# Kernel optimization log

Measured on AMD Instinct MI355X. Metric: run time of the kernel, lower is better.

## Reference

```python
import jax, jax.numpy as jnp
import numpy as np

N = 8192       # nodes == in_channels (diff matrix is NxN)
DF = 256       # feature dim of z
E = 65536      # edges (unused by forward, kept for signature fidelity)
M = 4096       # len(reliable_negatives)
NEG = 10       # neg_samples
STEPS = 10     # num_diffusion_steps
TEMP = 0.2


def setup_inputs() -> dict:
    key = jax.random.key(0)
    k1, k2, k3, k4, k5 = jax.random.split(key, 5)
    z = jax.random.normal(k1, (N, DF), dtype=jnp.float32)
    # learned parameter; init positive-uniform so row sums are well conditioned
    diff_matrix = jax.random.uniform(k2, (N, N), dtype=jnp.float32)
    edge_index = jax.random.randint(k3, (2, E), 0, N)
    reliable_negatives = jax.random.randint(k4, (M,), 0, N)
    # deterministic stand-in for torch.randint(0, len(reliable_negatives), (neg_samples,))
    neg_idx = jax.random.randint(k5, (NEG,), 0, M)
    return {"z": z, "diff_matrix": diff_matrix, "edge_index": edge_index,
            "reliable_negatives": reliable_negatives, "neg_idx": neg_idx}


def _l2norm(x):
    # F.normalize(dim=1): divide by L2 norm clamped at 1e-12
    n = jnp.sqrt(jnp.sum(x * x, axis=1, keepdims=True))
    return x / jnp.maximum(n, 1e-12)


def reference(z, diff_matrix, edge_index, reliable_negatives, neg_idx):
    # 10-step loop: mm(inverse(diag(rowsum)), M) == row-wise reciprocal scaling
    dm = diff_matrix
    for _ in range(STEPS):
        dm = dm / jnp.sum(dm, axis=1, keepdims=True)  # [N, N]
    # (normalized_diff_matrix with +eps*I is computed in the original but unused)

    anchor = z                       # [N, DF]
    positive = dm @ z                # [N, DF] diffused features
    negative = z[neg_idx]            # [NEG, DF]

    a = _l2norm(anchor)
    p = _l2norm(positive)
    n = _l2norm(negative)

    pos_sim = jnp.sum(a * p, axis=1) / TEMP                 # [N]
    neg_sim = jnp.exp(jnp.einsum('nd,kd->nk', a, n) / TEMP)  # [N, NEG]
    loss = -jnp.log(jnp.exp(pos_sim) / (jnp.exp(pos_sim) + neg_sim.sum(axis=1))).mean()
    return loss
```

## Files before the change

kernel.cpp:

```cpp
#include <hip/hip_runtime.h>
#include <hip/hip_bf16.h>


typedef float f32x4 __attribute__((ext_vector_type(4)));
typedef short s16x8 __attribute__((ext_vector_type(8)));

#define NN 8192
#define DFF 256
#define NNEG 10

__device__ __forceinline__ unsigned short f2bf(float x) {
  return __builtin_bit_cast(unsigned short, __float2bfloat16(x));
}

__device__ __forceinline__ float bf2f(unsigned short u) {
  return __builtin_bit_cast(float, (unsigned int)u << 16);
}

__device__ __forceinline__ void gload_lds16(const void* g, void* l) {
  __builtin_amdgcn_global_load_lds(
      (const __attribute__((address_space(1))) void*)(void*)g,
      (__attribute__((address_space(3))) void*)l, 16, 0, 0);
}

__device__ __forceinline__ float dot4(float4 a, float4 b) {
  return a.x * b.x + a.y * b.y + a.z * b.z + a.w * b.w;
}

__global__ void k_pack(const float* __restrict__ z,
                       unsigned short* __restrict__ zp) {
  __shared__ float tile[64][65];
  const int bx = blockIdx.x;
  const int by = blockIdx.y;
  const int t = threadIdx.x;
  const int lc = t & 63, lq = t >> 6;
#pragma unroll
  for (int p = 0; p < 16; ++p) {
    const int kr = lq * 16 + p;
    tile[kr][lc] = z[(size_t)(bx * 64 + kr) * DFF + by * 64 + lc];
  }
  __syncthreads();
#pragma unroll
  for (int p2 = 0; p2 < 2; ++p2) {
    const int ko = lq * 2 + p2;
    s16x8 v;
#pragma unroll
    for (int ke = 0; ke < 8; ++ke) v[ke] = (short)f2bf(tile[ko * 8 + ke][lc]);
    const int chunk = bx * 2 + (ko >> 2);
    const int kw = ko & 3;
    const int d = by * 64 + lc;
    *(s16x8*)(zp + (size_t)chunk * 8192 + kw * 2048 + d * 8) = v;
  }
}

__global__ __launch_bounds__(1024, 1) void k_gemm(const float* __restrict__ dm,
                                                  const unsigned short* __restrict__ zp,
                                                  unsigned short* __restrict__ part,
                                                  int KS) {
  __shared__ __align__(16) unsigned short sA[2][8192];
  __shared__ __align__(16) unsigned short sB[2][8192];
  const int bx = blockIdx.x;
  const int ks = bx & (KS - 1);
  const int mtile = bx / KS;
  const int klen = NN / KS;
  const int k0 = ks * klen;
  const int c0 = k0 >> 5;
  const int steps = klen / 32;
  const int tid = threadIdx.x;
  const int w = tid >> 6;
  const int l = tid & 63;
  const int m0 = mtile * 256;

  const int arow = tid >> 2;
  const int akw = tid & 3;
  const float* asrc = dm + (size_t)(m0 + arow) * NN + k0 + akw * 8;

  const int r16 = l & 15, kw = l >> 4;
  const int wm = w >> 2, wn = w & 3;

  f32x4 acc[4][4] = {};
  f32x4 a0, a1;

#define LOAD_A(t_)                                                           \
  {                                                                          \
    a0 = *(const f32x4*)(asrc + (t_)*32);                                    \
    a1 = *(const f32x4*)(asrc + (t_)*32 + 4);                                \
  }

#define WRITE_A(s_)                                                         \
  {                                                                         \
    s16x8 h_;                                                               \
    h_[0] = (short)f2bf(a0[0]); h_[1] = (short)f2bf(a0[1]);                 \
    h_[2] = (short)f2bf(a0[2]); h_[3] = (short)f2bf(a0[3]);                 \
    h_[4] = (short)f2bf(a1[0]); h_[5] = (short)f2bf(a1[1]);                 \
    h_[6] = (short)f2bf(a1[2]); h_[7] = (short)f2bf(a1[3]);                 \
    *(s16x8*)&sA[s_][akw * 2048 + arow * 8] = h_;                           \
  }

#define STAGE_B(t_, s_)                                                     \
  {                                                                         \
    const unsigned short* cs_ = zp + (size_t)(c0 + (t_)) * 8192;            \
    gload_lds16((const char*)(cs_ + w * 512) + l * 16,                      \
                (char*)sB[s_] + w * 1024);                                  \
  }

#define COMPUTE(s_)                                                         \
  {                                                                         \
    s16x8 af[4], bfr[4];                                                    \
    _Pragma("unroll") for (int mi = 0; mi < 4; ++mi) {                      \
      const int row_ = wm * 64 + mi * 16 + r16;                             \
      af[mi] = *(const s16x8*)&sA[s_][kw * 2048 + row_ * 8];                \
    }                                                                       \
    _Pragma("unroll") for (int nj = 0; nj < 4; ++nj) {                      \
      const int col_ = wn * 64 + nj * 16 + r16;                             \
      bfr[nj] = *(const s16x8*)&sB[s_][kw * 2048 + col_ * 8];               \
    }                                                                       \
    _Pragma("unroll") for (int mi = 0; mi < 4; ++mi)                        \
      _Pragma("unroll") for (int nj = 0; nj < 4; ++nj)                      \
        acc[mi][nj] = __builtin_amdgcn_mfma_f32_16x16x32_bf16(              \
            af[mi], bfr[nj], acc[mi][nj], 0, 0, 0);                         \
  }

  STAGE_B(0, 0);
  LOAD_A(0);
  WRITE_A(0);
  __syncthreads();

  for (int t = 0; t < steps; ++t) {
    const int cur = t & 1, nxt = cur ^ 1;
    if (t + 1 < steps) {
      LOAD_A(t + 1);
      STAGE_B(t + 1, nxt);
    }
    COMPUTE(cur);
    if (t + 1 < steps) WRITE_A(nxt);
    __syncthreads();
  }

#undef LOAD_A
#undef WRITE_A
#undef STAGE_B
#undef COMPUTE

  unsigned short* cb = part + (size_t)ks * NN * DFF;
#pragma unroll
  for (int mi = 0; mi < 4; ++mi)
#pragma unroll
    for (int nj = 0; nj < 4; ++nj) {
      const int col = wn * 64 + nj * 16 + r16;
      const int row0 = m0 + wm * 64 + mi * 16 + kw * 4;
#pragma unroll
      for (int r = 0; r < 4; ++r)
        cb[(size_t)(row0 + r) * DFF + col] = f2bf(acc[mi][nj][r]);
    }
}

__global__ __launch_bounds__(256) void k_loss(const float* __restrict__ z,
                                              const unsigned short* __restrict__ part,
                                              const int* __restrict__ neg_idx,
                                              float* __restrict__ lpart, int KS) {
  __shared__ float sneg[NNEG * DFF];
  __shared__ float swsum[4];
  const int t = threadIdx.x;
  const int w = t >> 6, l = t & 63;
  for (int k = w; k < NNEG; k += 4) {
    const int idx = neg_idx[k];
    float4 v = *(const float4*)(z + (size_t)idx * DFF + l * 4);
    float ss = dot4(v, v);
#pragma unroll
    for (int off = 32; off > 0; off >>= 1) ss += __shfl_xor(ss, off);
    const float s = 1.0f / fmaxf(sqrtf(ss), 1e-12f);
    float4 o;
    o.x = v.x * s; o.y = v.y * s; o.z = v.z * s; o.w = v.w * s;
    *(float4*)&sneg[k * DFF + l * 4] = o;
  }
  __syncthreads();
  const int gw = blockIdx.x * 4 + w;
  float lsum = 0.f;
  for (int rr = 0; rr < 8; ++rr) {
    const int i = gw * 8 + rr;
    const float4 a = *(const float4*)(z + (size_t)i * DFF + l * 4);
    float4 p; p.x = 0.f; p.y = 0.f; p.z = 0.f; p.w = 0.f;
    for (int ksp = 0; ksp < KS; ++ksp) {
      const ushort4 q =
          *(const ushort4*)(part + ((size_t)ksp * NN + i) * DFF + l * 4);
      p.x += bf2f(q.x); p.y += bf2f(q.y); p.z += bf2f(q.z); p.w += bf2f(q.w);
    }
    float vals[13];
    vals[0] = dot4(a, a);
    vals[1] = dot4(p, p);
    vals[2] = dot4(a, p);
#pragma unroll
    for (int k = 0; k < NNEG; ++k) {
      const float4 nv = *(const float4*)&sneg[k * DFF + l * 4];
      vals[3 + k] = dot4(a, nv);
    }
#pragma unroll
    for (int off = 32; off > 0; off >>= 1)
#pragma unroll
      for (int j = 0; j < 13; ++j) vals[j] += __shfl_xor(vals[j], off);
    const float na = fmaxf(sqrtf(vals[0]), 1e-12f);
    const float npp = fmaxf(sqrtf(vals[1]), 1e-12f);
    const float ps = vals[2] / (na * npp) * 5.0f;
    float S = 0.f;
#pragma unroll
    for (int k = 0; k < NNEG; ++k) S += expf(vals[3 + k] / na * 5.0f);
    lsum += logf(expf(ps) + S) - ps;
  }
  if (l == 0) swsum[w] = lsum;
  __syncthreads();
  if (t == 0) lpart[blockIdx.x] = swsum[0] + swsum[1] + swsum[2] + swsum[3];
}

__global__ void k_final(const float* __restrict__ lpart, float* __restrict__ out) {
  const int t = threadIdx.x;
  float v = lpart[t] + lpart[t + 64] + lpart[t + 128] + lpart[t + 192];
#pragma unroll
  for (int off = 32; off > 0; off >>= 1) v += __shfl_xor(v, off);
  if (t == 0) out[0] = v * (1.0f / (float)NN);
}

extern "C" void kernel_launch(void* const* d_in, const int* in_sizes, int n_in,
                              void* d_out, int out_size, void* d_ws, size_t ws_size,
                              hipStream_t stream) {
  const float* z = (const float*)d_in[0];
  const float* dm = (const float*)d_in[1];
  const int* neg_idx = (const int*)d_in[4];
  float* out = (float*)d_out;

  const size_t ZP = (size_t)NN * DFF * 2;
  auto need = [ZP](size_t ks) { return ZP + ks * (size_t)NN * DFF * 2 + 1024; };
  int KS = 8;
  if (ws_size < need(8)) KS = (ws_size >= need(4)) ? 4 : 2;

  char* ws = (char*)d_ws;
  unsigned short* zp = (unsigned short*)ws;
  unsigned short* part = (unsigned short*)(ws + ZP);
  float* lpart = (float*)(ws + ZP + (size_t)KS * NN * DFF * 2);

  k_pack<<<dim3(128, 4), 256, 0, stream>>>(z, zp);
  k_gemm<<<32 * KS, 1024, 0, stream>>>(dm, zp, part, KS);
  k_loss<<<256, 256, 0, stream>>>(z, part, neg_idx, lpart, KS);
  k_final<<<1, 64, 0, stream>>>(lpart, out);
}
```

Baseline: 130.9 us.

## Halve GEMM M-tile and assign K-splits per XCC via atomic work counter

The GEMM block tile shrinks from 256 to 128 rows with 512 threads and two blocks per CU, doubling the grid. Each block now takes its (mtile, k-split) from an atomic counter keyed by the hardware XCC id, so blocks on the same XCC tend to share the same K slice of the packed z operand and reuse it in that XCC's L2. The counters are zeroed in the pack kernel. This adds an atomic and a barrier at block start, and a fallback path that can give duplicate or missing tiles if counters overflow under odd scheduling.

```diff
diff --git a/kernel.cpp b/kernel.cpp
--- a/kernel.cpp
+++ b/kernel.cpp
@@ -28,7 +28,10 @@
 }
 
 __global__ void k_pack(const float* __restrict__ z,
-                       unsigned short* __restrict__ zp) {
+                       unsigned short* __restrict__ zp,
+                       unsigned int* __restrict__ cnt) {
+  if (blockIdx.x == 0 && blockIdx.y == 0 && threadIdx.x < 16)
+    cnt[threadIdx.x] = 0u;
   __shared__ float tile[64][65];
   const int bx = blockIdx.x;
   const int by = blockIdx.y;
@@ -53,15 +56,30 @@
   }
 }
 
-__global__ __launch_bounds__(1024, 1) void k_gemm(const float* __restrict__ dm,
-                                                  const unsigned short* __restrict__ zp,
-                                                  unsigned short* __restrict__ part,
-                                                  int KS) {
-  __shared__ __align__(16) unsigned short sA[2][8192];
+__global__ __launch_bounds__(512, 2) void k_gemm(const float* __restrict__ dm,
+                                                 const unsigned short* __restrict__ zp,
+                                                 unsigned short* __restrict__ part,
+                                                 unsigned int* __restrict__ cnt,
+                                                 int KS) {
+  __shared__ __align__(16) unsigned short sA[2][4096];
   __shared__ __align__(16) unsigned short sB[2][8192];
-  const int bx = blockIdx.x;
-  const int ks = bx & (KS - 1);
-  const int mtile = bx / KS;
+  __shared__ int s_mt, s_ks;
+  if (threadIdx.x == 0) {
+    unsigned int xcc;
+    asm volatile("s_getreg_b32 %0, hwreg(HW_REG_XCC_ID)" : "=s"(xcc));
+    xcc &= 7u;
+    int mt = 0, kk = 0;
+    for (int tr = 0; tr < 8; ++tr) {
+      const int k2 = (int)((xcc + (unsigned)tr) % (unsigned)KS);
+      const unsigned int o = atomicAdd(&cnt[k2], 1u);
+      if (o < 64u) { mt = (int)o; kk = k2; break; }
+    }
+    s_mt = mt;
+    s_ks = kk;
+  }
+  __syncthreads();
+  const int mtile = s_mt;
+  const int ks = s_ks;
   const int klen = NN / KS;
   const int k0 = ks * klen;
   const int c0 = k0 >> 5;
@@ -69,10 +87,10 @@
   const int tid = threadIdx.x;
   const int w = tid >> 6;
   const int l = tid & 63;
-  const int m0 = mtile * 256;
-
-  const int arow = tid >> 2;
-  const int akw = tid & 3;
+  const int m0 = mtile * 128;
+
+  const int arow = w * 16 + (l & 15);
+  const int akw = l >> 4;
   const float* asrc = dm + (size_t)(m0 + arow) * NN + k0 + akw * 8;
 
   const int r16 = l & 15, kw = l >> 4;
@@ -94,14 +112,17 @@
     h_[2] = (short)f2bf(a0[2]); h_[3] = (short)f2bf(a0[3]);                 \
     h_[4] = (short)f2bf(a1[0]); h_[5] = (short)f2bf(a1[1]);                 \
     h_[6] = (short)f2bf(a1[2]); h_[7] = (short)f2bf(a1[3]);                 \
-    *(s16x8*)&sA[s_][akw * 2048 + arow * 8] = h_;                           \
+    *(s16x8*)&sA[s_][akw * 1024 + arow * 8] = h_;                           \
   }
 
 #define STAGE_B(t_, s_)                                                     \
   {                                                                         \
     const unsigned short* cs_ = zp + (size_t)(c0 + (t_)) * 8192;            \
-    gload_lds16((const char*)(cs_ + w * 512) + l * 16,                      \
-                (char*)sB[s_] + w * 1024);                                  \
+    _Pragma("unroll") for (int q = 0; q < 2; ++q) {                         \
+      const int piece_ = w * 2 + q;                    \
+      gload_lds16((const char*)(cs_ + piece_ * 512) + l * 16,               \
+                  (char*)sB[s_] + piece_ * 1024);                           \
+    }                                                                       \
   }
 
 #define COMPUTE(s_)                                                         \
@@ -109,7 +130,7 @@
     s16x8 af[4], bfr[4];                                                    \
     _Pragma("unroll") for (int mi = 0; mi < 4; ++mi) {                      \
       const int row_ = wm * 64 + mi * 16 + r16;                             \
-      af[mi] = *(const s16x8*)&sA[s_][kw * 2048 + row_ * 8];                \
+      af[mi] = *(const s16x8*)&sA[s_][kw * 1024 + row_ * 8];                \
     }                                                                       \
     _Pragma("unroll") for (int nj = 0; nj < 4; ++nj) {                      \
       const int col_ = wn * 64 + nj * 16 + r16;                             \
@@ -229,7 +250,9 @@
   float* out = (float*)d_out;
 
   const size_t ZP = (size_t)NN * DFF * 2;
-  auto need = [ZP](size_t ks) { return ZP + ks * (size_t)NN * DFF * 2 + 1024; };
+  auto need = [ZP](size_t ks) {
+    return ZP + ks * (size_t)NN * DFF * 2 + 1024 + 64;
+  };
   int KS = 8;
   if (ws_size < need(8)) KS = (ws_size >= need(4)) ? 4 : 2;
 
@@ -237,9 +260,10 @@
   unsigned short* zp = (unsigned short*)ws;
   unsigned short* part = (unsigned short*)(ws + ZP);
   float* lpart = (float*)(ws + ZP + (size_t)KS * NN * DFF * 2);
-
-  k_pack<<<dim3(128, 4), 256, 0, stream>>>(z, zp);
-  k_gemm<<<32 * KS, 1024, 0, stream>>>(dm, zp, part, KS);
+  unsigned int* cnt = (unsigned int*)(ws + ZP + (size_t)KS * NN * DFF * 2 + 1024);
+
+  k_pack<<<dim3(128, 4), 256, 0, stream>>>(z, zp, cnt);
+  k_gemm<<<64 * KS, 512, 0, stream>>>(dm, zp, part, cnt, KS);
   k_loss<<<256, 256, 0, stream>>>(z, part, neg_idx, lpart, KS);
   k_final<<<1, 64, 0, stream>>>(lpart, out);
 }
```

Result: faster. 127.5 us (-2.6%).

## Shrink GEMM tiles to 128 rows and load B fragments directly from global

Applied to the files above, without the earlier changes.

The GEMM block shrinks from 1024 threads with a 256-row M tile to 512 threads with a 128-row tile. Four blocks per CU are allowed, the grid doubles, and the launch order becomes mtile-major. B fragments are no longer staged in LDS through global_load_lds; each wave reads its bf16 B fragments straight from global memory (L2-resident packed z), which halves LDS use and drops one LDS round trip. B loads now have no prefetch, so global latency is exposed in each step unless other blocks hide it. B is also re-read by more blocks.

```diff
diff --git a/kernel.cpp b/kernel.cpp
--- a/kernel.cpp
+++ b/kernel.cpp
@@ -15,12 +15,6 @@
 
 __device__ __forceinline__ float bf2f(unsigned short u) {
   return __builtin_bit_cast(float, (unsigned int)u << 16);
-}
-
-__device__ __forceinline__ void gload_lds16(const void* g, void* l) {
-  __builtin_amdgcn_global_load_lds(
-      (const __attribute__((address_space(1))) void*)(void*)g,
-      (__attribute__((address_space(3))) void*)l, 16, 0, 0);
 }
 
 __device__ __forceinline__ float dot4(float4 a, float4 b) {
@@ -53,15 +47,14 @@
   }
 }
 
-__global__ __launch_bounds__(1024, 1) void k_gemm(const float* __restrict__ dm,
-                                                  const unsigned short* __restrict__ zp,
-                                                  unsigned short* __restrict__ part,
-                                                  int KS) {
-  __shared__ __align__(16) unsigned short sA[2][8192];
-  __shared__ __align__(16) unsigned short sB[2][8192];
+__global__ __launch_bounds__(512, 4) void k_gemm(const float* __restrict__ dm,
+                                                 const unsigned short* __restrict__ zp,
+                                                 unsigned short* __restrict__ part,
+                                                 int KS) {
+  __shared__ __align__(16) unsigned short sA[2][4096];
   const int bx = blockIdx.x;
-  const int ks = bx & (KS - 1);
-  const int mtile = bx / KS;
+  const int mtile = bx & 63;
+  const int ks = bx >> 6;
   const int klen = NN / KS;
   const int k0 = ks * klen;
   const int c0 = k0 >> 5;
@@ -69,17 +62,27 @@
   const int tid = threadIdx.x;
   const int w = tid >> 6;
   const int l = tid & 63;
-  const int m0 = mtile * 256;
-
-  const int arow = tid >> 2;
-  const int akw = tid & 3;
+  const int m0 = mtile * 128;
+
+  const int arow = w * 16 + (l & 15);
+  const int akw = l >> 4;
   const float* asrc = dm + (size_t)(m0 + arow) * NN + k0 + akw * 8;
 
   const int r16 = l & 15, kw = l >> 4;
   const int wm = w >> 2, wn = w & 3;
 
+  const unsigned short* bbase = zp + (size_t)c0 * 8192 + kw * 2048 + (wn * 64 + r16) * 8;
+
   f32x4 acc[4][4] = {};
   f32x4 a0, a1;
+  s16x8 bfr[4];
+
+#define LOAD_B(t_)                                                           \
+  {                                                                          \
+    const unsigned short* bp_ = bbase + (size_t)(t_)*8192;                   \
+    _Pragma("unroll") for (int nj = 0; nj < 4; ++nj)                         \
+        bfr[nj] = *(const s16x8*)(bp_ + nj * 128);                           \
+  }
 
 #define LOAD_A(t_)                                                           \
   {                                                                          \
@@ -94,26 +97,15 @@
     h_[2] = (short)f2bf(a0[2]); h_[3] = (short)f2bf(a0[3]);                 \
     h_[4] = (short)f2bf(a1[0]); h_[5] = (short)f2bf(a1[1]);                 \
     h_[6] = (short)f2bf(a1[2]); h_[7] = (short)f2bf(a1[3]);                 \
-    *(s16x8*)&sA[s_][akw * 2048 + arow * 8] = h_;                           \
-  }
-
-#define STAGE_B(t_, s_)                                                     \
-  {                                                                         \
-    const unsigned short* cs_ = zp + (size_t)(c0 + (t_)) * 8192;            \
-    gload_lds16((const char*)(cs_ + w * 512) + l * 16,                      \
-                (char*)sB[s_] + w * 1024);                                  \
+    *(s16x8*)&sA[s_][akw * 1024 + arow * 8] = h_;                           \
   }
 
 #define COMPUTE(s_)                                                         \
   {                                                                         \
-    s16x8 af[4], bfr[4];                                                    \
+    s16x8 af[4];                                                            \
     _Pragma("unroll") for (int mi = 0; mi < 4; ++mi) {                      \
       const int row_ = wm * 64 + mi * 16 + r16;                             \
-      af[mi] = *(const s16x8*)&sA[s_][kw * 2048 + row_ * 8];                \
-    }                                                                       \
-    _Pragma("unroll") for (int nj = 0; nj < 4; ++nj) {                      \
-      const int col_ = wn * 64 + nj * 16 + r16;                             \
-      bfr[nj] = *(const s16x8*)&sB[s_][kw * 2048 + col_ * 8];               \
+      af[mi] = *(const s16x8*)&sA[s_][kw * 1024 + row_ * 8];                \
     }                                                                       \
     _Pragma("unroll") for (int mi = 0; mi < 4; ++mi)                        \
       _Pragma("unroll") for (int nj = 0; nj < 4; ++nj)                      \
@@ -121,25 +113,22 @@
             af[mi], bfr[nj], acc[mi][nj], 0, 0, 0);                         \
   }
 
-  STAGE_B(0, 0);
   LOAD_A(0);
   WRITE_A(0);
   __syncthreads();
 
   for (int t = 0; t < steps; ++t) {
     const int cur = t & 1, nxt = cur ^ 1;
-    if (t + 1 < steps) {
-      LOAD_A(t + 1);
-      STAGE_B(t + 1, nxt);
-    }
+    LOAD_B(t);
+    if (t + 1 < steps) LOAD_A(t + 1);
     COMPUTE(cur);
     if (t + 1 < steps) WRITE_A(nxt);
     __syncthreads();
   }
 
+#undef LOAD_B
 #undef LOAD_A
 #undef WRITE_A
-#undef STAGE_B
 #undef COMPUTE
 
   unsigned short* cb = part + (size_t)ks * NN * DFF;
@@ -239,7 +228,7 @@
   float* lpart = (float*)(ws + ZP + (size_t)KS * NN * DFF * 2);
 
   k_pack<<<dim3(128, 4), 256, 0, stream>>>(z, zp);
-  k_gemm<<<32 * KS, 1024, 0, stream>>>(dm, zp, part, KS);
+  k_gemm<<<64 * KS, 512, 0, stream>>>(dm, zp, part, KS);
   k_loss<<<256, 256, 0, stream>>>(z, part, neg_idx, lpart, KS);
   k_final<<<1, 64, 0, stream>>>(lpart, out);
 }
```

New measurement: 159.3 us. 1.22x slower.
